# Kernel optimization log

Measured on AMD Instinct MI355X. Metric: run time of the kernel, lower is better.

The kernel has to match this reference:

```python
import jax, jax.numpy as jnp
import numpy as np

N_EMBD = 1024
N_HEAD = 16


def setup_inputs() -> dict:
    key = jax.random.key(0)
    ks = jax.random.split(key, 11)
    B, T, T2, C = 4, 2048, 1024, N_EMBD
    s = 0.02
    return {
        "x": jax.random.normal(ks[0], (B, T, C), jnp.float32),
        "enc_x": jax.random.normal(ks[1], (B, T2, C), jnp.float32),
        "Wq": jax.random.normal(ks[2], (C, C), jnp.float32) * s,
        "bq": jax.random.normal(ks[3], (C,), jnp.float32) * s,
        "Wk": jax.random.normal(ks[4], (C, C), jnp.float32) * s,
        "bk": jax.random.normal(ks[5], (C,), jnp.float32) * s,
        "Wv": jax.random.normal(ks[6], (C, C), jnp.float32) * s,
        "bv": jax.random.normal(ks[7], (C,), jnp.float32) * s,
        "Wo": jax.random.normal(ks[8], (C, C), jnp.float32) * s,
        "bo": jax.random.normal(ks[9], (C,), jnp.float32) * s,
    }


def reference(x, enc_x, Wq, bq, Wk, bk, Wv, bv, Wo, bo):
    B, T, C = x.shape
    B2, T2, C2 = enc_x.shape
    H = N_HEAD
    D = C // H  # head dim
    q = x @ Wq + bq          # [B,T,C]
    k = enc_x @ Wk + bk      # [B,T2,C]
    v = enc_x @ Wv + bv      # [B,T2,C]
    q = q.reshape(B, T, H, D).transpose(0, 2, 1, 3)    # [B,H,T,D]
    k = k.reshape(B2, T2, H, D).transpose(0, 2, 1, 3)  # [B,H,T2,D]
    v = v.reshape(B2, T2, H, D).transpose(0, 2, 1, 3)  # [B,H,T2,D]
    att = jnp.einsum("bhtd,bhsd->bhts", q, k) * (1.0 / jnp.sqrt(jnp.float32(D)))
    att = jax.nn.softmax(att, axis=-1)                 # [B,H,T,T2]
    y = jnp.einsum("bhts,bhsd->bhtd", att, v)          # [B,H,T,D]
    y = y.transpose(0, 2, 1, 3).reshape(B, T, C)
    return y @ Wo + bo
```

## Files before the change

### kernel.cpp

```cpp
#include <hip/hip_runtime.h>
#include <hip/hip_bf16.h>


typedef __bf16 bf16_t;
typedef __bf16 bf16x8 __attribute__((ext_vector_type(8)));
typedef float f32x4 __attribute__((ext_vector_type(4)));
typedef float f32x16 __attribute__((ext_vector_type(16)));
typedef unsigned int u32x4 __attribute__((ext_vector_type(4)));

#define AS1C(p) ((const __attribute__((address_space(1))) void*)(p))
#define AS3(p)  ((__attribute__((address_space(3))) void*)(p))

constexpr int CC  = 1024;
constexpr int TT  = 2048;
constexpr int TT2 = 1024;

#if __has_builtin(__builtin_amdgcn_exp2f)
__device__ __forceinline__ float EXP2(float x) { return __builtin_amdgcn_exp2f(x); }
#else
__device__ __forceinline__ float EXP2(float x) { return exp2f(x); }
#endif

__global__ __launch_bounds__(256) void prep(const float* __restrict__ x, bf16_t* __restrict__ xb,
                                            const float* __restrict__ enc, bf16_t* __restrict__ eb,
                                            const float* __restrict__ W0, const float* __restrict__ W1,
                                            const float* __restrict__ W2, const float* __restrict__ W3,
                                            bf16_t* __restrict__ T0, bf16_t* __restrict__ T1,
                                            bf16_t* __restrict__ T2, bf16_t* __restrict__ T3) {
    __shared__ float tile[32][33];
    const int bid = blockIdx.x;
    if (bid < 2048) {
        int t = bid * 256 + threadIdx.x;
        #pragma unroll
        for (int k = 0; k < 3; ++k) {
            int i = t + k * 524288;
            const float* in; bf16_t* out; int j;
            if (i < 1048576) { in = x;   out = xb; j = i; }
            else             { in = enc; out = eb; j = i - 1048576; }
            const float4* p = (const float4*)in + 2 * (size_t)j;
            float4 a = p[0], b = p[1];
            bf16x8 v;
            v[0] = (bf16_t)a.x; v[1] = (bf16_t)a.y; v[2] = (bf16_t)a.z; v[3] = (bf16_t)a.w;
            v[4] = (bf16_t)b.x; v[5] = (bf16_t)b.y; v[6] = (bf16_t)b.z; v[7] = (bf16_t)b.w;
            *(bf16x8*)(out + (size_t)j * 8) = v;
        }
    } else {
        int idx = bid - 2048;
        int bx = idx & 31, by = (idx >> 5) & 31, bz = idx >> 10;
        const float* W; bf16_t* Tt;
        switch (bz) {
            case 0:  W = W0; Tt = T0; break;
            case 1:  W = W1; Tt = T1; break;
            case 2:  W = W2; Tt = T2; break;
            default: W = W3; Tt = T3; break;
        }
        int xx = threadIdx.x & 31, yy = threadIdx.x >> 5;
        int bxe = bx * 32, bye = by * 32;
        for (int i = 0; i < 4; ++i) {
            int r = yy + i * 8;
            tile[r][xx] = W[(size_t)(bye + r) * 1024 + bxe + xx];
        }
        __syncthreads();
        for (int i = 0; i < 4; ++i) {
            int r = yy + i * 8;
            Tt[(size_t)(bxe + r) * 1024 + bye + xx] = (bf16_t)tile[xx][r];
        }
    }
}


#define SB0 __builtin_amdgcn_sched_barrier(0)
#define GLL(src, dst) __builtin_amdgcn_global_load_lds(AS1C(src), AS3(dst), 16, 0, 0)

__device__ __forceinline__ bf16x8 ldx(const char* p) { return *(const bf16x8*)p; }

__global__ __launch_bounds__(512, 2) void gemm_qkv8(const bf16_t* __restrict__ xb,
                                                    const bf16_t* __restrict__ eb,
                                                    const bf16_t* __restrict__ wtq,
                                                    const bf16_t* __restrict__ wtk,
                                                    const float* __restrict__ bq,
                                                    const float* __restrict__ bk,
                                                    const float* __restrict__ bv,
                                                    bf16_t* __restrict__ Qs,
                                                    bf16_t* __restrict__ Ks,
                                                    bf16_t* __restrict__ Vs,
                                                    float qscale) {
    __shared__ __align__(16) char GLDS[131072];
    char* ldsA = &GLDS[0];
    char* ldsB = &GLDS[65536];

    const int tid = threadIdx.x;
    const int w   = tid >> 6;
    const int l   = tid & 63;
    const int wm  = w >> 2;
    const int wn  = w & 3;
    const int l15 = l & 15, lhi = l >> 4;

    const int bid = blockIdx.x;
    const bf16_t* Ap; const bf16_t* Bp;
    int m0, n0;
    float scale;
    const float* bias; bf16_t* outp; int outn0;
    bool vout = false;
    if (bid < 128) {
        int xcd = bid & 7, j = bid >> 3;
        n0 = (j & 3) * 256; m0 = (xcd * 4 + (j >> 2)) * 256;
        Ap = xb; Bp = wtq; scale = qscale;
        bias = bq; outp = Qs; outn0 = n0;
    } else {
        int b2 = bid - 128;
        int xcd = b2 & 7, j = b2 >> 3;
        n0 = (j & 7) * 256; m0 = (xcd * 2 + (j >> 3)) * 256;
        Ap = eb; Bp = wtk; scale = 1.0f;
        if (n0 < 1024) { bias = bk; outp = Ks; outn0 = n0; }
        else           { bias = bv; outp = Vs; outn0 = n0 - 1024; vout = true; }
    }

    const int lrow  = l >> 3;
    const int lslot = (l & 7) ^ lrow;
    const char* Asrc = (const char*)(Ap + (size_t)(m0 + w * 16 + lrow) * 1024 + lslot * 8);
    const char* Bsrc = (const char*)(Bp + (size_t)(n0 + w * 16 + lrow) * 1024 + lslot * 8);
    #define STG_A(t, buf, h)                                                                   \
        do {                                                                                   \
            GLL(Asrc + (size_t)(h) * 262144 + (t) * 128,         ldsA + (buf) * 32768 + (h) * 16384 + w * 2048);        \
            GLL(Asrc + (size_t)(h) * 262144 + 16384 + (t) * 128, ldsA + (buf) * 32768 + (h) * 16384 + w * 2048 + 1024); \
        } while (0)
    #define STG_B(t, buf, h)                                                                   \
        do {                                                                                   \
            GLL(Bsrc + (size_t)(h) * 262144 + (t) * 128,         ldsB + (buf) * 32768 + (h) * 16384 + w * 2048);        \
            GLL(Bsrc + (size_t)(h) * 262144 + 16384 + (t) * 128, ldsB + (buf) * 32768 + (h) * 16384 + w * 2048 + 1024); \
        } while (0)

    const int aoff = (wm * 128 + l15) * 128;
    const int boff = (wn * 64 + l15) * 128;
    const int sl0  = ((0 + lhi) ^ (l15 & 7)) << 4;
    const int sl1  = ((4 + lhi) ^ (l15 & 7)) << 4;

    #define RD_A(dst, KA, qm)                                                    \
        do { _Pragma("unroll") for (int mf = 0; mf < 4; ++mf) {                  \
            dst[mf * 2 + 0] = ldx((KA) + aoff + ((qm) * 64 + mf * 16) * 128 + sl0); \
            dst[mf * 2 + 1] = ldx((KA) + aoff + ((qm) * 64 + mf * 16) * 128 + sl1); } } while (0)
    #define RD_B(dst, KB, qn)                                                    \
        do { _Pragma("unroll") for (int nf = 0; nf < 2; ++nf) {                  \
            dst[nf * 2 + 0] = ldx((KB) + boff + ((qn) * 32 + nf * 16) * 128 + sl0); \
            dst[nf * 2 + 1] = ldx((KB) + boff + ((qn) * 32 + nf * 16) * 128 + sl1); } } while (0)

    #define MFMA16(qm, qn, Af, Bf)                                                             \
        do { __builtin_amdgcn_s_setprio(1);                                                    \
            _Pragma("unroll") for (int mf = 0; mf < 4; ++mf)                                   \
            _Pragma("unroll") for (int nf = 0; nf < 2; ++nf) {                                 \
                acc[(qm) * 4 + mf][(qn) * 2 + nf] = __builtin_amdgcn_mfma_f32_16x16x32_bf16(   \
                    Af[mf * 2 + 0], Bf[nf * 2 + 0], acc[(qm) * 4 + mf][(qn) * 2 + nf], 0, 0, 0); \
                acc[(qm) * 4 + mf][(qn) * 2 + nf] = __builtin_amdgcn_mfma_f32_16x16x32_bf16(   \
                    Af[mf * 2 + 1], Bf[nf * 2 + 1], acc[(qm) * 4 + mf][(qn) * 2 + nf], 0, 0, 0); } \
            __builtin_amdgcn_s_setprio(0); } while (0)

    #define PH_BAR do { SB0; __builtin_amdgcn_s_barrier(); SB0;                                \
                        asm volatile("s_waitcnt lgkmcnt(0)" ::: "memory"); SB0; } while (0)
    #define PH_END do { SB0; __builtin_amdgcn_s_barrier(); SB0; } while (0)

    f32x4 acc[8][4] = {};
    bf16x8 A0[8], A1[8], B0[4], B1[4];

    STG_A(0, 0, 0); STG_A(0, 0, 1);
    STG_B(0, 0, 0); STG_B(0, 0, 1);
    STG_A(1, 1, 0); STG_A(1, 1, 1);
    asm volatile("s_waitcnt vmcnt(4)" ::: "memory");
    SB0; __builtin_amdgcn_s_barrier(); SB0;

    constexpr int NT = 16;
    for (int t = 0; t < NT; ++t) {
        const int buf = t & 1;
        const char* KA = ldsA + buf * 32768;
        const char* KB = ldsB + buf * 32768;

        if (t + 1 < NT) STG_B(t + 1, buf ^ 1, 0);
        RD_A(A0, KA, 0); RD_B(B0, KB, 0);
        PH_BAR;
        MFMA16(0, 0, A0, B0);
        PH_END;

        if (t + 1 < NT) STG_B(t + 1, buf ^ 1, 1);
        RD_A(A1, KA, 1);
        PH_BAR;
        MFMA16(1, 0, A1, B0);
        PH_END;

        if (t + 2 < NT) STG_A(t + 2, buf, 0);
        RD_B(B1, KB, 1);
        PH_BAR;
        MFMA16(1, 1, A1, B1);
        PH_END;

        if (t + 2 < NT) STG_A(t + 2, buf, 1);
        SB0; __builtin_amdgcn_s_barrier(); SB0;
        MFMA16(0, 1, A0, B1);
        if (t < NT - 2) asm volatile("s_waitcnt vmcnt(4)" ::: "memory");
        else            asm volatile("s_waitcnt vmcnt(0)" ::: "memory");
        PH_END;
    }

    __syncthreads();
    char* EP = GLDS + w * 16384;

    if (!vout) {
        #pragma unroll
        for (int ni = 0; ni < 4; ++ni) {
            int c_rel = ni * 16 + l15;
            float bvv = bias[outn0 + wn * 64 + c_rel];
            #pragma unroll
            for (int mi = 0; mi < 8; ++mi) {
                int mbase = mi * 16 + lhi * 4;
                #pragma unroll
                for (int r = 0; r < 4; ++r)
                    *(bf16_t*)(EP + (mbase + r) * 128 + c_rel * 2) =
                        (bf16_t)((acc[mi][ni][r] + bvv) * scale);
            }
        }
        asm volatile("s_waitcnt lgkmcnt(0)" ::: "memory");
        SB0;
        char* gbase = (char*)outp + (size_t)(m0 + wm * 128) * 2048 + (outn0 + wn * 64) * 2;
        #pragma unroll
        for (int i = 0; i < 16; ++i) {
            int m_rel = i * 8 + (l >> 3);
            int ch = l & 7;
            bf16x8 v = *(const bf16x8*)(EP + m_rel * 128 + ch * 16);
            *(bf16x8*)(gbase + (size_t)m_rel * 2048 + ch * 16) = v;
        }
    } else {
        int col0 = outn0 + wn * 64;
        int hh = col0 >> 6;
        int rowbase = m0 + wm * 128;
        int bb = rowbase >> 10, key0 = rowbase & 1023;
        #pragma unroll
        for (int ni = 0; ni < 4; ++ni) {
            int dd = ni * 16 + l15;
            float bvv = bias[col0 + dd];
            int sw = (dd & 7) << 4;
            #pragma unroll
            for (int mi = 0; mi < 8; ++mi) {
                int kb = mi * 16 + lhi * 4;
                #pragma unroll
                for (int r = 0; r < 4; ++r)
                    *(bf16_t*)(EP + dd * 256 + (((kb + r) * 2) ^ sw)) =
                        (bf16_t)((acc[mi][ni][r] + bvv) * scale);
            }
        }
        asm volatile("s_waitcnt lgkmcnt(0)" ::: "memory");
        SB0;
        char* gbase = (char*)outp + ((size_t)((bb * 16 + hh) * 64) * 1024 + key0) * 2;
        #pragma unroll
        for (int i = 0; i < 16; ++i) {
            int dd = i * 4 + (l >> 4);
            int ch = l & 15;
            bf16x8 v = *(const bf16x8*)(EP + dd * 256 + ((ch * 16) ^ ((dd & 7) << 4)));
            *(bf16x8*)(gbase + (size_t)dd * 2048 + ch * 16) = v;
        }
    }
    #undef STG_A
    #undef STG_B
    #undef RD_A
    #undef RD_B
    #undef MFMA16
    #undef PH_BAR
    #undef PH_END
}

__device__ __forceinline__ void gemm_body(bf16_t* As, bf16_t* Bs,
                                          const bf16_t* __restrict__ A,
                                          const bf16_t* __restrict__ Bt,
                                          const float* __restrict__ bias,
                                          float* __restrict__ out,
                                          int lgNT, int mband, int bid) {
    const int tid  = threadIdx.x;
    const int lane = tid & 63;
    const int wave = tid >> 6;
    const int wr = wave >> 1, wc = wave & 1;
    const int l15 = lane & 15, lhi = lane >> 4;

    const int xcd = bid & 7;
    const int j   = bid >> 3;
    const int n0  = (j & ((1 << lgNT) - 1)) * 128;
    const int m0  = (xcd * mband + (j >> lgNT)) * 128;

    f32x4 acc[4][4] = {};

    for (int k0 = 0; k0 < 1024; k0 += 32) {
        for (int i = 0; i < 2; ++i) {
            int e   = i * 2048 + wave * 512 + lane * 8;
            int row = e >> 5, col = e & 31;
            __builtin_amdgcn_global_load_lds(AS1C(A  + (size_t)(m0 + row) * 1024 + k0 + col),
                                             AS3(As + i * 2048 + wave * 512), 16, 0, 0);
            __builtin_amdgcn_global_load_lds(AS1C(Bt + (size_t)(n0 + row) * 1024 + k0 + col),
                                             AS3(Bs + i * 2048 + wave * 512), 16, 0, 0);
        }
        __syncthreads();
        bf16x8 a[4], b[4];
        #pragma unroll
        for (int m = 0; m < 4; ++m)
            a[m] = *(const bf16x8*)&As[(wr * 64 + m * 16 + l15) * 32 + lhi * 8];
        #pragma unroll
        for (int n = 0; n < 4; ++n)
            b[n] = *(const bf16x8*)&Bs[(wc * 64 + n * 16 + l15) * 32 + lhi * 8];
        #pragma unroll
        for (int m = 0; m < 4; ++m)
            #pragma unroll
            for (int n = 0; n < 4; ++n)
                acc[m][n] = __builtin_amdgcn_mfma_f32_16x16x32_bf16(a[m], b[n], acc[m][n], 0, 0, 0);
        __syncthreads();
    }

    #pragma unroll
    for (int n = 0; n < 4; ++n) {
        int col = n0 + wc * 64 + n * 16 + l15;
        float bv = bias[col];
        #pragma unroll
        for (int m = 0; m < 4; ++m) {
            int rowb = m0 + wr * 64 + m * 16 + lhi * 4;
            #pragma unroll
            for (int r = 0; r < 4; ++r)
                out[(size_t)(rowb + r) * 1024 + col] = acc[m][n][r] + bv;
        }
    }
}

__global__ __launch_bounds__(256) void gemm_out(const bf16_t* __restrict__ yb,
                                                const bf16_t* __restrict__ wto,
                                                const float* __restrict__ bo,
                                                float* __restrict__ out) {
    __shared__ __align__(16) bf16_t As[128 * 32];
    __shared__ __align__(16) bf16_t Bs[128 * 32];
    gemm_body(As, Bs, yb, wto, bo, out, 3, 8, blockIdx.x);
}

__device__ __forceinline__ unsigned pk_bf16(float lo, float hi) {
    unsigned r;
    asm("v_cvt_pk_bf16_f32 %0, %1, %2" : "=v"(r) : "v"(lo), "v"(hi));
    return r;
}
__device__ __forceinline__ void swap32(unsigned &a, unsigned &b) {
    asm("v_permlane32_swap_b32 %0, %1" : "+v"(a), "+v"(b));
}
__device__ __forceinline__ float sum_halves(float x) {
    unsigned a = __builtin_bit_cast(unsigned, x), b = a;
    swap32(a, b);
    return __builtin_bit_cast(float, a) + __builtin_bit_cast(float, b);
}
__device__ __forceinline__ bf16x8 ldsf(const bf16_t* base, int row, int colb) {
    int off = row * 128 + (colb ^ ((row & 7) << 4));
    return *(const bf16x8*)((const char*)base + off);
}
__device__ __forceinline__ bf16x8 packP(const f32x16& s0, const f32x16& s1, int kt) {
    const f32x16& sp = (kt < 2) ? s0 : s1;
    const int rb = (kt & 1) * 8;
    unsigned a0 = pk_bf16(sp[rb + 0], sp[rb + 1]);
    unsigned a1 = pk_bf16(sp[rb + 2], sp[rb + 3]);
    unsigned a2 = pk_bf16(sp[rb + 4], sp[rb + 5]);
    unsigned a3 = pk_bf16(sp[rb + 6], sp[rb + 7]);
    swap32(a0, a2);
    swap32(a1, a3);
    union { u32x4 u; bf16x8 h; } cv;
    cv.u = (u32x4){a0, a1, a2, a3};
    return cv.h;
}

__global__ __launch_bounds__(256, 2) void attn256(const bf16_t* __restrict__ Q,
                                                  const bf16_t* __restrict__ K,
                                                  const bf16_t* __restrict__ Vt,
                                                  bf16_t* __restrict__ Y) {
    __shared__ __align__(16) bf16_t SM[3][2][64 * 64];

    const int tid = threadIdx.x;
    const int l   = tid & 63;
    const int w   = tid >> 6;
    const int l31 = l & 31;
    const int lh  = l >> 5;

    const int bid = blockIdx.x;
    const int bh  = bid & 63;
    const int qb  = bid >> 6;
    const int b = bh >> 4, h = bh & 15;
    const int q0 = qb * 256 + w * 64;

    const bf16_t* Qb = Q + (size_t)b * TT * CC + h * 64;
    const char* Kc = (const char*)(K + (size_t)b * TT2 * CC + h * 64);
    const char* Vc = (const char*)(Vt + (size_t)bh * 64 * 1024);

    bf16x8 qfA[4], qfB[4];
    #pragma unroll
    for (int kt = 0; kt < 4; ++kt) {
        qfA[kt] = *(const bf16x8*)&Qb[(size_t)(q0 + l31)      * CC + kt * 16 + lh * 8];
        qfB[kt] = *(const bf16x8*)&Qb[(size_t)(q0 + 32 + l31) * CC + kt * 16 + lh * 8];
    }
    __builtin_amdgcn_sched_barrier(0);

    f32x16 yA0 = {}, yA1 = {}, yB0 = {}, yB1 = {};
    float lsA = 0.f, lsB = 0.f;

    const int krow = w * 16 + (l >> 3);
    const int ss   = ((l & 7) ^ (l >> 3)) & 7;
    const int off0 = krow * 2048 + ss * 16;
    const int off1 = off0 + 8 * 2048;

    #define STAGE(t, buf)                                                                 \
        do {                                                                              \
            __builtin_amdgcn_global_load_lds(AS1C(Kc + (size_t)(t) * 131072 + off0),      \
                                             AS3((char*)&SM[buf][0][0] + w * 2048), 16, 0, 0);        \
            __builtin_amdgcn_global_load_lds(AS1C(Kc + (size_t)(t) * 131072 + off1),      \
                                             AS3((char*)&SM[buf][0][0] + w * 2048 + 1024), 16, 0, 0); \
            __builtin_amdgcn_global_load_lds(AS1C(Vc + (t) * 128 + off0),                 \
                                             AS3((char*)&SM[buf][1][0] + w * 2048), 16, 0, 0);        \
            __builtin_amdgcn_global_load_lds(AS1C(Vc + (t) * 128 + off1),                 \
                                             AS3((char*)&SM[buf][1][0] + w * 2048 + 1024), 16, 0, 0); \
        } while (0)

    #define SUMEXP(s0, s1, ls)                                                    \
        do {                                                                      \
            float rs = 0.f;                                                       \
            _Pragma("unroll")                                                     \
            for (int r = 0; r < 16; ++r) {                                        \
                s0[r] = EXP2(s0[r]);                                              \
                s1[r] = EXP2(s1[r]);                                              \
                rs += s0[r] + s1[r];                                              \
            }                                                                     \
            ls += sum_halves(rs);                                                 \
        } while (0)

    constexpr int NT = TT2 / 64;
    STAGE(0, 0);
    STAGE(1, 1);

    int cur = 0;
    for (int t = 0; t < NT; ++t) {
        if (t + 1 < NT) asm volatile("s_waitcnt vmcnt(4)" ::: "memory");
        else            asm volatile("s_waitcnt vmcnt(0)" ::: "memory");
        __builtin_amdgcn_sched_barrier(0);
        __builtin_amdgcn_s_barrier();
        __builtin_amdgcn_sched_barrier(0);

        if (t + 2 < NT) {
            int nb = cur + 2; if (nb >= 3) nb -= 3;
            STAGE(t + 2, nb);
        }

        const bf16_t* Kl = &SM[cur][0][0];
        const bf16_t* Vl = &SM[cur][1][0];

        f32x16 sA0 = {}, sA1 = {}, sB0 = {}, sB1 = {};
        #pragma unroll
        for (int kt = 0; kt < 4; ++kt) {
            int colb = kt * 32 + (lh << 4);
            bf16x8 a0 = ldsf(Kl, l31,      colb);
            bf16x8 a1 = ldsf(Kl, 32 + l31, colb);
            sA0 = __builtin_amdgcn_mfma_f32_32x32x16_bf16(a0, qfA[kt], sA0, 0, 0, 0);
            sB0 = __builtin_amdgcn_mfma_f32_32x32x16_bf16(a0, qfB[kt], sB0, 0, 0, 0);
            sA1 = __builtin_amdgcn_mfma_f32_32x32x16_bf16(a1, qfA[kt], sA1, 0, 0, 0);
            sB1 = __builtin_amdgcn_mfma_f32_32x32x16_bf16(a1, qfB[kt], sB1, 0, 0, 0);
        }

        SUMEXP(sA0, sA1, lsA);
        SUMEXP(sB0, sB1, lsB);

        __builtin_amdgcn_s_setprio(1);
        #pragma unroll
        for (int kt = 0; kt < 4; ++kt) {
            bf16x8 pA = packP(sA0, sA1, kt);
            bf16x8 pB = packP(sB0, sB1, kt);
            int colb = kt * 32 + (lh << 4);
            bf16x8 v0 = ldsf(Vl, l31,      colb);
            bf16x8 v1 = ldsf(Vl, 32 + l31, colb);
            yA0 = __builtin_amdgcn_mfma_f32_32x32x16_bf16(v0, pA, yA0, 0, 0, 0);
            yA1 = __builtin_amdgcn_mfma_f32_32x32x16_bf16(v1, pA, yA1, 0, 0, 0);
            yB0 = __builtin_amdgcn_mfma_f32_32x32x16_bf16(v0, pB, yB0, 0, 0, 0);
            yB1 = __builtin_amdgcn_mfma_f32_32x32x16_bf16(v1, pB, yB1, 0, 0, 0);
        }
        __builtin_amdgcn_s_setprio(0);

        ++cur; if (cur == 3) cur = 0;
    }
    #undef STAGE
    #undef SUMEXP

    __syncthreads();

    float iA = 1.f / lsA, iB = 1.f / lsB;
    char* ob = (char*)&SM[0][0][0] + w * 8192;
    const int sw = (l31 & 7) << 4;
    #pragma unroll
    for (int r = 0; r < 16; ++r) {
        int drow = (r & 3) + 8 * (r >> 2) + 4 * lh;
        *(bf16_t*)(ob + l31 * 128 + ((drow * 2) ^ sw))               = (bf16_t)(yA0[r] * iA);
        *(bf16_t*)(ob + l31 * 128 + (((32 + drow) * 2) ^ sw))        = (bf16_t)(yA1[r] * iA);
        *(bf16_t*)(ob + 4096 + l31 * 128 + ((drow * 2) ^ sw))        = (bf16_t)(yB0[r] * iB);
        *(bf16_t*)(ob + 4096 + l31 * 128 + (((32 + drow) * 2) ^ sw)) = (bf16_t)(yB1[r] * iB);
    }
    __syncthreads();
    bf16_t* Yb = Y + (size_t)b * TT * CC + h * 64 + (size_t)q0 * CC;
    #pragma unroll
    for (int i = 0; i < 8; ++i) {
        int qr = i * 8 + (l >> 3);
        int c  = ((l & 7) * 16) ^ ((qr & 7) << 4);
        bf16x8 v = *(const bf16x8*)(ob + (qr >> 5) * 4096 + (qr & 31) * 128 + c);
        *(bf16x8*)&Yb[(size_t)qr * CC + (l & 7) * 8] = v;
    }
}

extern "C" void kernel_launch(void* const* d_in, const int* in_sizes, int n_in,
                              void* d_out, int out_size, void* d_ws, size_t ws_size,
                              hipStream_t stream) {
    const float* x   = (const float*)d_in[0];
    const float* enc = (const float*)d_in[1];
    const float* Wq  = (const float*)d_in[2];
    const float* bq  = (const float*)d_in[3];
    const float* Wk  = (const float*)d_in[4];
    const float* bk  = (const float*)d_in[5];
    const float* Wv  = (const float*)d_in[6];
    const float* bv  = (const float*)d_in[7];
    const float* Wo  = (const float*)d_in[8];
    const float* bo  = (const float*)d_in[9];

    char* w = (char*)d_ws;
    size_t o = 0;
    bf16_t* xb  = (bf16_t*)(w + o); o += (size_t)8192 * 1024 * 2;
    bf16_t* eb  = (bf16_t*)(w + o); o += (size_t)4096 * 1024 * 2;
    bf16_t* wtq = (bf16_t*)(w + o); o += (size_t)1024 * 1024 * 2;
    bf16_t* wtk = (bf16_t*)(w + o); o += (size_t)1024 * 1024 * 2;
    bf16_t* wtv = (bf16_t*)(w + o); o += (size_t)1024 * 1024 * 2;
    bf16_t* wto = (bf16_t*)(w + o); o += (size_t)1024 * 1024 * 2;
    bf16_t* Qs  = (bf16_t*)(w + o); o += (size_t)8192 * 1024 * 2;
    bf16_t* Ks  = (bf16_t*)(w + o); o += (size_t)4096 * 1024 * 2;
    bf16_t* Vt  = (bf16_t*)(w + o); o += (size_t)4096 * 1024 * 2;
    bf16_t* yb  = (bf16_t*)(w + o); o += (size_t)8192 * 1024 * 2;

    prep<<<6144, 256, 0, stream>>>(x, xb, enc, eb, Wq, Wk, Wv, Wo, wtq, wtk, wtv, wto);

    const float qscale = 0.125f * 1.4426950408889634f;
    gemm_qkv8<<<256, 512, 0, stream>>>(xb, eb, wtq, wtk, bq, bk, bv, Qs, Ks, Vt, qscale);

    attn256<<<512, 256, 0, stream>>>(Qs, Ks, Vt, yb);

    gemm_out<<<512, 256, 0, stream>>>(yb, wto, bo, (float*)d_out);
}
```

Measured before the change: 118.7 us.

## Software-pipeline attention loop: compute next QK^T before current softmax-PV

```diff
diff --git a/kernel.cpp b/kernel.cpp
--- a/kernel.cpp
+++ b/kernel.cpp
@@ -67,7 +67,6 @@
         }
     }
 }
-
 
 #define SB0 __builtin_amdgcn_sched_barrier(0)
 #define GLL(src, dst) __builtin_amdgcn_global_load_lds(AS1C(src), AS3(dst), 16, 0, 0)
@@ -426,60 +425,73 @@
             ls += sum_halves(rs);                                                 \
         } while (0)
 
+    #define QKT(Sa0, Sa1, Sb0, Sb1, Kl)                                           \
+        do {                                                                      \
+            Sa0 = (f32x16){}; Sa1 = (f32x16){};                                   \
+            Sb0 = (f32x16){}; Sb1 = (f32x16){};                                   \
+            _Pragma("unroll")                                                     \
+            for (int kt = 0; kt < 4; ++kt) {                                      \
+                int colb = kt * 32 + (lh << 4);                                   \
+                bf16x8 a0 = ldsf((Kl), l31,      colb);                           \
+                bf16x8 a1 = ldsf((Kl), 32 + l31, colb);                           \
+                Sa0 = __builtin_amdgcn_mfma_f32_32x32x16_bf16(a0, qfA[kt], Sa0, 0, 0, 0); \
+                Sb0 = __builtin_amdgcn_mfma_f32_32x32x16_bf16(a0, qfB[kt], Sb0, 0, 0, 0); \
+                Sa1 = __builtin_amdgcn_mfma_f32_32x32x16_bf16(a1, qfA[kt], Sa1, 0, 0, 0); \
+                Sb1 = __builtin_amdgcn_mfma_f32_32x32x16_bf16(a1, qfB[kt], Sb1, 0, 0, 0); \
+            }                                                                     \
+        } while (0)
+
+    #define SMPV(Sa0, Sa1, Sb0, Sb1, Vl)                                          \
+        do {                                                                      \
+            SUMEXP(Sa0, Sa1, lsA);                                                \
+            SUMEXP(Sb0, Sb1, lsB);                                                \
+            __builtin_amdgcn_s_setprio(1);                                        \
+            _Pragma("unroll")                                                     \
+            for (int kt = 0; kt < 4; ++kt) {                                      \
+                bf16x8 pA = packP(Sa0, Sa1, kt);                                  \
+                bf16x8 pB = packP(Sb0, Sb1, kt);                                  \
+                int colb = kt * 32 + (lh << 4);                                   \
+                bf16x8 v0 = ldsf((Vl), l31,      colb);                           \
+                bf16x8 v1 = ldsf((Vl), 32 + l31, colb);                           \
+                yA0 = __builtin_amdgcn_mfma_f32_32x32x16_bf16(v0, pA, yA0, 0, 0, 0); \
+                yA1 = __builtin_amdgcn_mfma_f32_32x32x16_bf16(v1, pA, yA1, 0, 0, 0); \
+                yB0 = __builtin_amdgcn_mfma_f32_32x32x16_bf16(v0, pB, yB0, 0, 0, 0); \
+                yB1 = __builtin_amdgcn_mfma_f32_32x32x16_bf16(v1, pB, yB1, 0, 0, 0); \
+            }                                                                     \
+            __builtin_amdgcn_s_setprio(0);                                        \
+        } while (0)
+
+    #define ITER(Ca0, Ca1, Cb0, Cb1, Na0, Na1, Nb0, Nb1, t, bc, bn, bs)           \
+        do {                                                                      \
+            asm volatile("s_waitcnt vmcnt(0)" ::: "memory");                      \
+            SB0; __builtin_amdgcn_s_barrier(); SB0;                               \
+            if ((t) + 2 < NT) STAGE((t) + 2, bs);                                 \
+            if ((t) + 1 < NT) QKT(Na0, Na1, Nb0, Nb1, &SM[bn][0][0]);             \
+            SMPV(Ca0, Ca1, Cb0, Cb1, &SM[bc][1][0]);                              \
+        } while (0)
+
     constexpr int NT = TT2 / 64;
+    f32x16 sXa0, sXa1, sXb0, sXb1, sYa0, sYa1, sYb0, sYb1;
+
     STAGE(0, 0);
     STAGE(1, 1);
-
-    int cur = 0;
-    for (int t = 0; t < NT; ++t) {
-        if (t + 1 < NT) asm volatile("s_waitcnt vmcnt(4)" ::: "memory");
-        else            asm volatile("s_waitcnt vmcnt(0)" ::: "memory");
-        __builtin_amdgcn_sched_barrier(0);
-        __builtin_amdgcn_s_barrier();
-        __builtin_amdgcn_sched_barrier(0);
-
-        if (t + 2 < NT) {
-            int nb = cur + 2; if (nb >= 3) nb -= 3;
-            STAGE(t + 2, nb);
-        }
-
-        const bf16_t* Kl = &SM[cur][0][0];
-        const bf16_t* Vl = &SM[cur][1][0];
-
-        f32x16 sA0 = {}, sA1 = {}, sB0 = {}, sB1 = {};
-        #pragma unroll
-        for (int kt = 0; kt < 4; ++kt) {
-            int colb = kt * 32 + (lh << 4);
-            bf16x8 a0 = ldsf(Kl, l31,      colb);
-            bf16x8 a1 = ldsf(Kl, 32 + l31, colb);
-            sA0 = __builtin_amdgcn_mfma_f32_32x32x16_bf16(a0, qfA[kt], sA0, 0, 0, 0);
-            sB0 = __builtin_amdgcn_mfma_f32_32x32x16_bf16(a0, qfB[kt], sB0, 0, 0, 0);
-            sA1 = __builtin_amdgcn_mfma_f32_32x32x16_bf16(a1, qfA[kt], sA1, 0, 0, 0);
-            sB1 = __builtin_amdgcn_mfma_f32_32x32x16_bf16(a1, qfB[kt], sB1, 0, 0, 0);
-        }
-
-        SUMEXP(sA0, sA1, lsA);
-        SUMEXP(sB0, sB1, lsB);
-
-        __builtin_amdgcn_s_setprio(1);
-        #pragma unroll
-        for (int kt = 0; kt < 4; ++kt) {
-            bf16x8 pA = packP(sA0, sA1, kt);
-            bf16x8 pB = packP(sB0, sB1, kt);
-            int colb = kt * 32 + (lh << 4);
-            bf16x8 v0 = ldsf(Vl, l31,      colb);
-            bf16x8 v1 = ldsf(Vl, 32 + l31, colb);
-            yA0 = __builtin_amdgcn_mfma_f32_32x32x16_bf16(v0, pA, yA0, 0, 0, 0);
-            yA1 = __builtin_amdgcn_mfma_f32_32x32x16_bf16(v1, pA, yA1, 0, 0, 0);
-            yB0 = __builtin_amdgcn_mfma_f32_32x32x16_bf16(v0, pB, yB0, 0, 0, 0);
-            yB1 = __builtin_amdgcn_mfma_f32_32x32x16_bf16(v1, pB, yB1, 0, 0, 0);
-        }
-        __builtin_amdgcn_s_setprio(0);
-
-        ++cur; if (cur == 3) cur = 0;
+    asm volatile("s_waitcnt vmcnt(4)" ::: "memory");
+    SB0; __builtin_amdgcn_s_barrier(); SB0;
+    QKT(sXa0, sXa1, sXb0, sXb1, &SM[0][0][0]);
+
+    int c0 = 0;
+    for (int t = 0; t < NT; t += 2) {
+        int c1 = c0 + 1; if (c1 == 3) c1 = 0;
+        int c2 = c1 + 1; if (c2 == 3) c2 = 0;
+        ITER(sXa0, sXa1, sXb0, sXb1, sYa0, sYa1, sYb0, sYb1, t,     c0, c1, c2);
+        ITER(sYa0, sYa1, sYb0, sYb1, sXa0, sXa1, sXb0, sXb1, t + 1, c1, c2, c0);
+        c0 = c2;
     }
     #undef STAGE
     #undef SUMEXP
+    #undef QKT
+    #undef SMPV
+    #undef ITER
 
     __syncthreads();
 
```

New measurement: 127.2 us. 1.07x slower.
